# Kernel tuning notes

Measured on AMD Instinct MI355X. Metric: run time of the kernel, lower is better.

## Reference

```python
import jax, jax.numpy as jnp
import numpy as np

B = 8192      # batch
F = 20        # sparse features
V = 1000      # vocab per sparse feature
E = 32        # embedding dim
ND = 10       # dense features
IN0 = (F + ND) * E  # 960 total embed dim
T = 2         # tasks
K = 4         # task experts per task
S = 4         # shared experts
D = 512       # expert dim
H = 256       # tower hidden
TEMP = 2.0    # gate temperature
EPS = 1e-5    # batchnorm eps


def setup_inputs() -> dict:
    key = jax.random.key(0)
    ks = iter(jax.random.split(key, 64))
    n = lambda shape, s=0.02: jax.random.normal(next(ks), shape, dtype=jnp.float32) * s
    inp = {
        'sparse_features': jax.random.randint(next(ks), (B, F), 0, V, dtype=jnp.int32),
        'dense_features': jax.random.normal(next(ks), (B, ND), dtype=jnp.float32),
        'emb_tables': n((F, V, E), 0.05),
        'dense_W': n((ND, ND * E)),
        'dense_b': jnp.zeros((ND * E,), jnp.float32),
    }
    for i, ind in enumerate([IN0, D, D]):
        inp[f'l{i}_Wt'] = n((T, K, ind, D))
        inp[f'l{i}_bt'] = jnp.zeros((T, K, D), jnp.float32)
        inp[f'l{i}_Ws'] = n((S, ind, D))
        inp[f'l{i}_bs'] = jnp.zeros((S, D), jnp.float32)
        inp[f'l{i}_Wg'] = n((T, ind, K + S))
        inp[f'l{i}_bg'] = jnp.zeros((T, K + S), jnp.float32)
    inp['tw1'] = n((T, D, H)); inp['tb1'] = jnp.zeros((T, H), jnp.float32)
    inp['bn_g'] = jnp.ones((T, H), jnp.float32); inp['bn_b'] = jnp.zeros((T, H), jnp.float32)
    inp['bn_m'] = jnp.zeros((T, H), jnp.float32); inp['bn_v'] = jnp.ones((T, H), jnp.float32)
    inp['tw2'] = n((T, H, H // 2)); inp['tb2'] = jnp.zeros((T, H // 2), jnp.float32)
    inp['tw3'] = n((T, H // 2)); inp['tb3'] = jnp.zeros((T,), jnp.float32)
    return inp


def _ple_layer(x, Wt, bt, Ws, bs, Wg, bg):
    # x: [B, in]; Wt: [T,K,in,D]; Ws: [S,in,D]; Wg: [T,in,K+S]
    shared = jax.nn.relu(jnp.einsum('bi,sio->bso', x, Ws) + bs)        # [B,S,D]
    task = jax.nn.relu(jnp.einsum('bi,tkio->btko', x, Wt) + bt)        # [B,T,K,D]
    Bn = x.shape[0]
    stack = jnp.concatenate(
        [task, jnp.broadcast_to(shared[:, None], (Bn, T) + shared.shape[1:])], axis=2)  # [B,T,K+S,D]
    gw = jax.nn.softmax((jnp.einsum('bi,tie->bte', x, Wg) + bg) / TEMP, axis=-1)        # [B,T,K+S]
    return jnp.einsum('bte,bted->btd', gw, stack)                      # [B,T,D]


def reference(sparse_features, dense_features, emb_tables, dense_W, dense_b,
              l0_Wt, l0_bt, l0_Ws, l0_bs, l0_Wg, l0_bg,
              l1_Wt, l1_bt, l1_Ws, l1_bs, l1_Wg, l1_bg,
              l2_Wt, l2_bt, l2_Ws, l2_bs, l2_Wg, l2_bg,
              tw1, tb1, bn_g, bn_b, bn_m, bn_v, tw2, tb2, tw3, tb3):
    # embedding: per-feature table lookup then concat with projected dense
    sp = emb_tables[jnp.arange(F)[None, :], sparse_features]           # [B,F,E]
    embed = jnp.concatenate(
        [sp.reshape(sp.shape[0], F * E), dense_features @ dense_W + dense_b], axis=1)  # [B,IN0]

    x = embed
    tout = None
    for (Wt, bt, Ws, bs, Wg, bg) in [
        (l0_Wt, l0_bt, l0_Ws, l0_bs, l0_Wg, l0_bg),
        (l1_Wt, l1_bt, l1_Ws, l1_bs, l1_Wg, l1_bg),
        (l2_Wt, l2_bt, l2_Ws, l2_bs, l2_Wg, l2_bg),
    ]:
        tout = _ple_layer(x, Wt, bt, Ws, bs, Wg, bg)   # [B,T,D]
        x = tout.mean(axis=1)                           # next layer input

    # task towers (eval mode: BN uses running stats, dropout off)
    h = jnp.einsum('btd,tdh->bth', tout, tw1) + tb1
    h = (h - bn_m) / jnp.sqrt(bn_v + EPS) * bn_g + bn_b
    h = jax.nn.relu(h)
    h = jax.nn.relu(jnp.einsum('bth,thg->btg', h, tw2) + tb2)
    logits = jnp.einsum('btg,tg->bt', h, tw3) + tb3     # [B,T]

    ctr = jax.nn.sigmoid(logits[:, 0])
    cvr_raw = jax.nn.sigmoid(logits[:, 1])
    ctcvr = ctr * cvr_raw
    # use_esmm=True -> cvr_pred == ctcvr
    return jnp.stack([ctr, ctcvr, ctcvr])               # [3,B]: ctr, cvr, ctcvr
```

## Files before the change

kernel.cpp:

```cpp
#include <hip/hip_runtime.h>
#include <math.h>

#define Bn 8192
#define INP0 960
#define Dn 512
#define Hn 256
#define TEMP_INV 0.5f

typedef __attribute__((ext_vector_type(8))) short short8;
typedef __attribute__((ext_vector_type(8))) unsigned short ushort8;
typedef __attribute__((ext_vector_type(4))) float f32x4;

__device__ __forceinline__ int swz(int x) { return x ^ ((x >> 3) & 0x70); }
__device__ __forceinline__ int swz8(int x) { return x ^ (((x >> 7) & 3) << 3); }

__device__ __forceinline__ unsigned short f2bf(float f) {
  unsigned u = __builtin_bit_cast(unsigned, f);
  u += 0x7FFF + ((u >> 16) & 1);
  return (unsigned short)(u >> 16);
}
__device__ __forceinline__ float bf2f(unsigned short s) {
  unsigned u = ((unsigned)s) << 16;
  return __builtin_bit_cast(float, u);
}
__device__ __forceinline__ int pk4fp8(float a, float b, float c, float d) {
  int r = __builtin_amdgcn_cvt_pk_fp8_f32(a, b, 0, 0);
  r = __builtin_amdgcn_cvt_pk_fp8_f32(c, d, r, 1);
  return r;
}
__device__ __forceinline__ void gload16(const void* g, void* l) {
  __builtin_amdgcn_global_load_lds(
      (const __attribute__((address_space(1))) unsigned int*)g,
      (__attribute__((address_space(3))) unsigned int*)l, 16, 0, 0);
}

template <int IN>
__global__ __launch_bounds__(256) void conv_w(const float* __restrict__ Wt,
                                              const float* __restrict__ Ws,
                                              unsigned char* __restrict__ Wbt) {
  __shared__ float T[64][33];
  const int NK = IN / 32;
  int kk = blockIdx.x, dblk = blockIdx.y, e = blockIdx.z;
  int t = threadIdx.x;
  const float* base = (e < 8) ? (Wt + (size_t)e * IN * Dn) : (Ws + (size_t)(e - 8) * IN * Dn);
  int k = t >> 3, dq = t & 7;
  const float* gp = base + (size_t)(kk * 32 + k) * Dn + dblk * 64 + dq * 8;
  float4 v0 = *(const float4*)gp, v1 = *(const float4*)(gp + 4);
  T[dq * 8 + 0][k] = v0.x; T[dq * 8 + 1][k] = v0.y; T[dq * 8 + 2][k] = v0.z; T[dq * 8 + 3][k] = v0.w;
  T[dq * 8 + 4][k] = v1.x; T[dq * 8 + 5][k] = v1.y; T[dq * 8 + 6][k] = v1.z; T[dq * 8 + 7][k] = v1.w;
  __syncthreads();
  int L = t * 8;
  int nat = swz8(L);
  int c = nat >> 5, k0 = nat & 31;
  int2 o;
  o.x = pk4fp8(T[c][k0 + 0] * 16.f, T[c][k0 + 1] * 16.f, T[c][k0 + 2] * 16.f, T[c][k0 + 3] * 16.f);
  o.y = pk4fp8(T[c][k0 + 4] * 16.f, T[c][k0 + 5] * 16.f, T[c][k0 + 6] * 16.f, T[c][k0 + 7] * 16.f);
  *(int2*)(Wbt + (((size_t)(dblk * NK + kk) * 12 + e) << 11) + L) = o;
}

template <int K, int H>
__global__ __launch_bounds__(256) void conv_tw(const float* __restrict__ W,
                                               unsigned short* __restrict__ out) {
  __shared__ float T[64][33];
  int kk = blockIdx.x, hb = blockIdx.y, t = blockIdx.z;
  int tid = threadIdx.x;
  const float* base = W + (size_t)t * K * H;
  int k = tid >> 3, dq = tid & 7;
  const float* gp = base + (size_t)(kk * 32 + k) * H + hb * 64 + dq * 8;
  float4 v0 = *(const float4*)gp, v1 = *(const float4*)(gp + 4);
  T[dq * 8 + 0][k] = v0.x; T[dq * 8 + 1][k] = v0.y; T[dq * 8 + 2][k] = v0.z; T[dq * 8 + 3][k] = v0.w;
  T[dq * 8 + 4][k] = v1.x; T[dq * 8 + 5][k] = v1.y; T[dq * 8 + 6][k] = v1.z; T[dq * 8 + 7][k] = v1.w;
  __syncthreads();
  int L = tid * 16;
  int nat = swz(L);
  int c = nat >> 6, k0 = (nat & 63) >> 1;
  ushort8 o;
#pragma unroll
  for (int u = 0; u < 8; ++u) o[u] = f2bf(T[c][k0 + u]);
  const int NHB = H / 64;
  *(ushort8*)(out + (((size_t)(kk * NHB + hb) * 2 + t) << 11) + (L >> 1)) = o;
}

__global__ __launch_bounds__(256) void embed_kernel(
    const int* __restrict__ sparse, const float* __restrict__ dense,
    const float* __restrict__ emb, const float* __restrict__ dW,
    const float* __restrict__ db,
    unsigned short* __restrict__ xn, unsigned char* __restrict__ xt) {
  int b = blockIdx.x, t = threadIdx.x;
  __shared__ float dfs[10];
  if (t < 10) dfs[t] = dense[b * 10 + t];
  __syncthreads();
  if (t >= 240) return;
  int c = t * 4;
  float v[4];
  if (c < 640) {
    int f = c >> 5, e0 = c & 31;
    int idx = sparse[b * 20 + f];
    const float* ep = emb + ((size_t)f * 1000 + idx) * 32 + e0;
    float4 q = *(const float4*)ep;
    v[0] = q.x; v[1] = q.y; v[2] = q.z; v[3] = q.w;
  } else {
    int j = c - 640;
#pragma unroll
    for (int u = 0; u < 4; ++u) {
      float a = db[j + u];
#pragma unroll
      for (int d = 0; d < 10; ++d) a += dfs[d] * dW[d * 320 + j + u];
      v[u] = a;
    }
  }
  ushort4 pk;
  pk.x = f2bf(v[0]); pk.y = f2bf(v[1]); pk.z = f2bf(v[2]); pk.w = f2bf(v[3]);
  *(ushort4*)(xn + (size_t)b * 960 + c) = pk;
  int kk = c >> 5, bblk = b >> 6;
  int nat = ((b & 63) << 5) + (c & 31);
  int p8 = pk4fp8(v[0] * 16.f, v[1] * 16.f, v[2] * 16.f, v[3] * 16.f);
  *(int*)(xt + (((size_t)kk * 128 + bblk) << 11) + swz8(nat)) = p8;
}

template <int IN>
__global__ __launch_bounds__(256) void gate_kernel(
    const unsigned short* __restrict__ x, const float* __restrict__ Wg,
    const float* __restrict__ bg, float* __restrict__ gates) {
  int tid = threadIdx.x;
  int wv = tid >> 6, lane = tid & 63;
  int b = blockIdx.x * 4 + wv;
  int e = lane & 15, t = e >> 3, eg = e & 7;
  int slice = lane >> 4;
  const unsigned short* xr = x + (size_t)b * IN;
  const float* wr = Wg + (size_t)t * IN * 8 + eg;
  float p = 0.f;
  for (int i = slice * (IN / 4); i < (slice + 1) * (IN / 4); i += 4) {
    ushort4 xv = *(const ushort4*)(xr + i);
    p += bf2f(xv.x) * wr[(size_t)(i + 0) * 8];
    p += bf2f(xv.y) * wr[(size_t)(i + 1) * 8];
    p += bf2f(xv.z) * wr[(size_t)(i + 2) * 8];
    p += bf2f(xv.w) * wr[(size_t)(i + 3) * 8];
  }
  p += __shfl_xor(p, 32);
  p += __shfl_xor(p, 16);
  float z = (p + bg[t * 8 + eg]) * TEMP_INV;
  float m = z;
  m = fmaxf(m, __shfl_xor(m, 1)); m = fmaxf(m, __shfl_xor(m, 2)); m = fmaxf(m, __shfl_xor(m, 4));
  float ex = expf(z - m);
  float s = ex;
  s += __shfl_xor(s, 1); s += __shfl_xor(s, 2); s += __shfl_xor(s, 4);
  if (lane < 16) gates[(size_t)b * 16 + lane] = ex / s;
}

#define GSH 0
#define OUTS 4096
#define SB 22528
#define STG 26624

template <int IN, int MODE>
__global__ __launch_bounds__(768, 3) void ple_mfma(
    const unsigned char* __restrict__ xt, const float* __restrict__ gates,
    const unsigned char* __restrict__ Wbt,
    const float* __restrict__ btb, const float* __restrict__ bsh,
    unsigned short* __restrict__ outn, unsigned char* __restrict__ outt8,
    unsigned short* __restrict__ outtb) {
  __shared__ __align__(16) char smem[102400];
  const int NKv = IN / 32;
  int tid = threadIdx.x;
  int wv = tid >> 6, lane = tid & 63;
  int r = lane & 15, g = lane >> 4;
  int s = blockIdx.x;
  int dblk = s & 7, bblk = s >> 3;
  int b0 = bblk * 64, d0 = dblk * 64;

  if (tid < 256)
    *(float4*)(smem + GSH + tid * 16) = *(const float4*)(gates + (size_t)b0 * 16 + tid * 4);

  f32x4 acc[4][4];
#pragma unroll
  for (int i = 0; i < 4; ++i)
#pragma unroll
    for (int j = 0; j < 4; ++j) acc[i][j] = f32x4{0.f, 0.f, 0.f, 0.f};

  const unsigned char* xchunk = xt + ((size_t)bblk << 11);
  const unsigned char* wchunk = Wbt + ((size_t)(dblk * NKv) * 12 << 11);

  auto stage = [&](int t, char* lb) {
    const unsigned char* ws = wchunk + (size_t)t * 24576;
    gload16(ws + tid * 16, lb + tid * 16);
    gload16(ws + tid * 16 + 12288, lb + tid * 16 + 12288);
    if (tid < 128)
      gload16(xchunk + (size_t)t * (128 * 2048) + tid * 16, lb + 24576 + tid * 16);
  };

  stage(0, smem + SB);
  stage(1, smem + SB + STG);

  for (int kk = 0; kk < NKv; ++kk) {
    if (kk == NKv - 1) {
      asm volatile("s_waitcnt vmcnt(0)" ::: "memory");
    } else if (tid < 128) {
      asm volatile("s_waitcnt vmcnt(3)" ::: "memory");
    } else {
      asm volatile("s_waitcnt vmcnt(2)" ::: "memory");
    }
    __builtin_amdgcn_s_barrier();
    {
      const char* lb = smem + SB + (kk % 3) * STG;
      const char* xb = lb + 24576;
      const char* wb = lb + (wv << 11);
      long A[4], B[4];
#pragma unroll
      for (int rt = 0; rt < 4; ++rt)
        A[rt] = *(const long*)(xb + swz8(((rt * 16 + r) << 5) + (g << 3)));
#pragma unroll
      for (int ct = 0; ct < 4; ++ct)
        B[ct] = *(const long*)(wb + swz8(((ct * 16 + r) << 5) + (g << 3)));
#pragma unroll
      for (int rt = 0; rt < 4; ++rt)
#pragma unroll
        for (int ct = 0; ct < 4; ++ct)
          acc[rt][ct] = __builtin_amdgcn_mfma_f32_16x16x32_fp8_fp8(A[rt], B[ct], acc[rt][ct], 0, 0, 0);
    }
    if (kk + 2 < NKv) stage(kk + 2, smem + SB + ((kk + 2) % 3) * STG);
  }
  __syncthreads();

  {
    const float* bp = (wv < 8) ? (btb + wv * Dn) : (bsh + (wv - 8) * Dn);
    float bias[4];
#pragma unroll
    for (int ct = 0; ct < 4; ++ct) bias[ct] = bp[d0 + ct * 16 + r];
    char* ex = smem + SB + (wv << 12);
#pragma unroll
    for (int rt = 0; rt < 4; ++rt)
#pragma unroll
      for (int ct = 0; ct < 4; ++ct) {
        float v0 = fmaxf(acc[rt][ct][0] * 0.00390625f + bias[ct], 0.f) * 16.f;
        float v1 = fmaxf(acc[rt][ct][1] * 0.00390625f + bias[ct], 0.f) * 16.f;
        float v2 = fmaxf(acc[rt][ct][2] * 0.00390625f + bias[ct], 0.f) * 16.f;
        float v3 = fmaxf(acc[rt][ct][3] * 0.00390625f + bias[ct], 0.f) * 16.f;
        int col = ct * 16 + r;
        int off = (col << 6) + rt * 16 + g * 4;
        off ^= (col & 7) << 3;
        *(int*)(ex + off) = pk4fp8(v0, v1, v2, v3);
      }
  }
  __syncthreads();

  if (tid < 512) {
    int col = tid & 63, q = tid >> 6;
    int exoff = ((col << 6) + (q << 3)) ^ ((col & 7) << 3);
    long v[12];
#pragma unroll
    for (int e = 0; e < 12; ++e)
      v[e] = *(const long*)(smem + SB + (e << 12) + exoff);
    unsigned short* os0 = (unsigned short*)(smem + OUTS);
    unsigned short* os1 = os0 + 64 * 72;
#pragma unroll
    for (int half = 0; half < 2; ++half) {
#pragma unroll
      for (int jj = 0; jj < 4; ++jj) {
        int row = (q << 3) + half * 4 + jj;
        const float* gp = (const float*)(smem + GSH + (row << 6));
        float4 ga = ((const float4*)gp)[0];
        float4 gb = ((const float4*)gp)[1];
        float4 gc = ((const float4*)gp)[2];
        float4 gd = ((const float4*)gp)[3];
        float f[12];
#pragma unroll
        for (int e = 0; e < 12; ++e) {
          unsigned w32 = (unsigned)(v[e] >> (half * 32));
          f[e] = __builtin_amdgcn_cvt_f32_fp8((int)(w32 >> (jj * 8)), 0);
        }
        float s0 = ga.x * f[0] + ga.y * f[1] + ga.z * f[2] + ga.w * f[3] +
                   gb.x * f[8] + gb.y * f[9] + gb.z * f[10] + gb.w * f[11];
        float s1 = gc.x * f[4] + gc.y * f[5] + gc.z * f[6] + gc.w * f[7] +
                   gd.x * f[8] + gd.y * f[9] + gd.z * f[10] + gd.w * f[11];
        os0[row * 72 + col] = f2bf(s0 * 0.0625f);
        os1[row * 72 + col] = f2bf(s1 * 0.0625f);
      }
    }
  }
  __syncthreads();

  if (tid < 512) {
    int row = tid >> 3, cq = tid & 7;
    const unsigned short* os0 = (const unsigned short*)(smem + OUTS) + row * 72 + cq * 8;
    const unsigned short* os1 = os0 + 64 * 72;
    ushort8 p0 = *(const ushort8*)os0, p1 = *(const ushort8*)os1;
    int b = b0 + row, d = d0 + cq * 8;
    int kk2 = d >> 5;
    if (MODE == 0) {
      float m[8];
      ushort8 pk;
#pragma unroll
      for (int u = 0; u < 8; ++u) {
        m[u] = 0.5f * (bf2f((unsigned short)p0[u]) + bf2f((unsigned short)p1[u]));
        pk[u] = f2bf(m[u]);
      }
      *(ushort8*)(outn + (size_t)b * Dn + d) = pk;
      int nat = (row << 5) + (d & 31);
      int2 o8;
      o8.x = pk4fp8(m[0] * 16.f, m[1] * 16.f, m[2] * 16.f, m[3] * 16.f);
      o8.y = pk4fp8(m[4] * 16.f, m[5] * 16.f, m[6] * 16.f, m[7] * 16.f);
      *(int2*)(outt8 + (((size_t)kk2 * 128 + bblk) << 11) + swz8(nat)) = o8;
    } else {
      int nat = (row << 6) + ((d & 31) << 1);
      *(ushort8*)(outtb + (((size_t)(0 * 16 + kk2) * 128 + bblk) << 11) + (swz(nat) >> 1)) = p0;
      *(ushort8*)(outtb + (((size_t)(1 * 16 + kk2) * 128 + bblk) << 11) + (swz(nat) >> 1)) = p1;
    }
  }
}

#define TWBUF 36864
#define H1OFF 73728

__global__ __launch_bounds__(512) void tower_mfma(
    const unsigned short* __restrict__ toutT,
    const unsigned short* __restrict__ twbt1, const unsigned short* __restrict__ twbt2,
    const float* __restrict__ tb1,
    const float* __restrict__ bng, const float* __restrict__ bnb,
    const float* __restrict__ bnm, const float* __restrict__ bnv,
    const float* __restrict__ tb2, const float* __restrict__ tw3,
    const float* __restrict__ tb3, float* __restrict__ out) {
  __shared__ __align__(16) char smem[106496];
  int tid = threadIdx.x;
  int wv = tid >> 6, lane = tid & 63, r = lane & 15, g = lane >> 4;
  int blk = blockIdx.x;
  int bblk = blk >> 1, sub = blk & 1;
  int b0 = blk * 32;
  char* h1t = smem + H1OFF;

  int t1 = wv >> 2, hb = wv & 3;
  f32x4 acc[2][4];
#pragma unroll
  for (int i = 0; i < 2; ++i)
#pragma unroll
    for (int j = 0; j < 4; ++j) acc[i][j] = f32x4{0.f, 0.f, 0.f, 0.f};

  auto stage1 = [&](int t, char* lb) {
#pragma unroll
    for (int i = 0; i < 4; ++i)
      gload16((const char*)twbt1 + (size_t)t * 32768 + tid * 16 + i * 8192,
              lb + tid * 16 + i * 8192);
    if (tid < 256) {
      int tt = tid >> 7, off = (tid & 127) * 16;
      gload16((const char*)toutT + (((size_t)(tt * 16 + t) * 128 + bblk) << 12) + sub * 2048 + off,
              lb + 32768 + tt * 2048 + off);
    }
  };

  stage1(0, smem);
  __syncthreads();
  int cur = 0;
  for (int kk = 0; kk < 16; ++kk) {
    if (kk + 1 < 16) stage1(kk + 1, smem + (cur ^ 1) * TWBUF);
    {
      const char* lb = smem + cur * TWBUF;
      const char* wb = lb + (hb * 2 + t1) * 4096;
      const char* xb = lb + 32768 + t1 * 2048;
      short8 a[2], bfr[4];
#pragma unroll
      for (int rt = 0; rt < 2; ++rt)
        a[rt] = *(const short8*)(xb + swz(((rt * 16 + r) << 6) + (g << 4)));
#pragma unroll
      for (int ct = 0; ct < 4; ++ct)
        bfr[ct] = *(const short8*)(wb + swz(((ct * 16 + r) << 6) + (g << 4)));
#pragma unroll
      for (int rt = 0; rt < 2; ++rt)
#pragma unroll
        for (int ct = 0; ct < 4; ++ct)
          acc[rt][ct] = __builtin_amdgcn_mfma_f32_16x16x32_bf16(a[rt], bfr[ct], acc[rt][ct], 0, 0, 0);
    }
    __syncthreads();
    cur ^= 1;
  }

  {
#pragma unroll
    for (int ct = 0; ct < 4; ++ct) {
      int h = hb * 64 + ct * 16 + r;
      int idx = t1 * 256 + h;
      float inv = rsqrtf(bnv[idx] + 1e-5f) * bng[idx];
      float mu = bnm[idx], be = bnb[idx], bias = tb1[idx];
      int kk2 = h >> 5, kloc = h & 31;
      char* tile = h1t + (t1 * 8 + kk2) * 2048;
#pragma unroll
      for (int rt = 0; rt < 2; ++rt)
#pragma unroll
        for (int j = 0; j < 4; ++j) {
          int lr = rt * 16 + g * 4 + j;
          float v = acc[rt][ct][j] + bias;
          v = (v - mu) * inv + be;
          v = fmaxf(v, 0.f);
          *(unsigned short*)(tile + swz((lr << 6) + (kloc << 1))) = f2bf(v);
        }
    }
  }
  __syncthreads();

  float* h2x = (float*)smem;
  if (wv < 4) {
    int t2 = wv >> 1, hb2 = wv & 1;
    f32x4 acc2[2][4];
#pragma unroll
    for (int i = 0; i < 2; ++i)
#pragma unroll
      for (int j = 0; j < 4; ++j) acc2[i][j] = f32x4{0.f, 0.f, 0.f, 0.f};
    for (int kk = 0; kk < 8; ++kk) {
      const char* xb = h1t + (t2 * 8 + kk) * 2048;
      const char* wb = (const char*)twbt2 + ((kk * 2 + hb2) * 2 + t2) * 4096;
      short8 a[2], bfr[4];
#pragma unroll
      for (int rt = 0; rt < 2; ++rt)
        a[rt] = *(const short8*)(xb + swz(((rt * 16 + r) << 6) + (g << 4)));
#pragma unroll
      for (int ct = 0; ct < 4; ++ct)
        bfr[ct] = *(const short8*)(wb + swz(((ct * 16 + r) << 6) + (g << 4)));
#pragma unroll
      for (int rt = 0; rt < 2; ++rt)
#pragma unroll
        for (int ct = 0; ct < 4; ++ct)
          acc2[rt][ct] = __builtin_amdgcn_mfma_f32_16x16x32_bf16(a[rt], bfr[ct], acc2[rt][ct], 0, 0, 0);
    }
#pragma unroll
    for (int ct = 0; ct < 4; ++ct) {
      int col = hb2 * 64 + ct * 16 + r;
      float bias = tb2[t2 * 128 + col];
#pragma unroll
      for (int rt = 0; rt < 2; ++rt)
#pragma unroll
        for (int j = 0; j < 4; ++j) {
          int lr = rt * 16 + g * 4 + j;
          h2x[(t2 * 32 + lr) * 129 + col] = fmaxf(acc2[rt][ct][j] + bias, 0.f);
        }
    }
  }
  __syncthreads();

  float* lgs = (float*)(smem + 40960);
  if (tid < 64) {
    int t3 = tid >> 5, lr = tid & 31;
    const float* hr = h2x + (t3 * 32 + lr) * 129;
    const float* w3 = tw3 + t3 * 128;
    float s = 0.f;
#pragma unroll 8
    for (int i = 0; i < 128; ++i) s += hr[i] * w3[i];
    lgs[t3 * 32 + lr] = s + tb3[t3];
  }
  __syncthreads();
  if (tid < 32) {
    int b = b0 + tid;
    float ctr = 1.f / (1.f + expf(-lgs[tid]));
    float cvr = 1.f / (1.f + expf(-lgs[32 + tid]));
    float cc = ctr * cvr;
    out[b] = ctr;
    out[Bn + b] = cc;
    out[2 * Bn + b] = cc;
  }
}

extern "C" void kernel_launch(void* const* d_in, const int* in_sizes, int n_in,
                              void* d_out, int out_size, void* d_ws, size_t ws_size,
                              hipStream_t stream) {
  const int* sparse   = (const int*)d_in[0];
  const float* dense  = (const float*)d_in[1];
  const float* emb    = (const float*)d_in[2];
  const float* dW     = (const float*)d_in[3];
  const float* db     = (const float*)d_in[4];
  const float* Wt[3]  = {(const float*)d_in[5],  (const float*)d_in[11], (const float*)d_in[17]};
  const float* btb[3] = {(const float*)d_in[6],  (const float*)d_in[12], (const float*)d_in[18]};
  const float* Wsh[3] = {(const float*)d_in[7],  (const float*)d_in[13], (const float*)d_in[19]};
  const float* bsh[3] = {(const float*)d_in[8],  (const float*)d_in[14], (const float*)d_in[20]};
  const float* Wg[3]  = {(const float*)d_in[9],  (const float*)d_in[15], (const float*)d_in[21]};
  const float* bg[3]  = {(const float*)d_in[10], (const float*)d_in[16], (const float*)d_in[22]};
  const float* tw1 = (const float*)d_in[23];
  const float* tb1 = (const float*)d_in[24];
  const float* bng = (const float*)d_in[25];
  const float* bnb = (const float*)d_in[26];
  const float* bnm = (const float*)d_in[27];
  const float* bnv = (const float*)d_in[28];
  const float* tw2 = (const float*)d_in[29];
  const float* tb2 = (const float*)d_in[30];
  const float* tw3 = (const float*)d_in[31];
  const float* tb3 = (const float*)d_in[32];

  unsigned short* x0n = (unsigned short*)d_ws;
  unsigned short* x1n = x0n + (size_t)Bn * 960;
  unsigned short* toutT = x1n + (size_t)Bn * 512;
  float* gatesB = (float*)(toutT + (size_t)Bn * 1024);
  unsigned short* twbt1 = (unsigned short*)(gatesB + (size_t)Bn * 16);
  unsigned short* twbt2 = twbt1 + (size_t)2 * 512 * 256;
  unsigned char* x0t = (unsigned char*)(twbt2 + (size_t)2 * 256 * 128);
  unsigned char* x1t = x0t + (size_t)Bn * 960;
  unsigned char* Wbt = x1t + (size_t)Bn * 512;
  unsigned short* x2n = x0n;
  unsigned char* x2t = x0t;

  conv_tw<512, 256><<<dim3(16, 4, 2), 256, 0, stream>>>(tw1, twbt1);
  conv_tw<256, 128><<<dim3(8, 2, 2), 256, 0, stream>>>(tw2, twbt2);

  conv_w<960><<<dim3(30, 8, 12), 256, 0, stream>>>(Wt[0], Wsh[0], Wbt);
  embed_kernel<<<Bn, 256, 0, stream>>>(sparse, dense, emb, dW, db, x0n, x0t);
  gate_kernel<960><<<Bn / 4, 256, 0, stream>>>(x0n, Wg[0], bg[0], gatesB);
  ple_mfma<960, 0><<<1024, 768, 0, stream>>>(x0t, gatesB, Wbt, btb[0], bsh[0], x1n, x1t, nullptr);

  conv_w<512><<<dim3(16, 8, 12), 256, 0, stream>>>(Wt[1], Wsh[1], Wbt);
  gate_kernel<512><<<Bn / 4, 256, 0, stream>>>(x1n, Wg[1], bg[1], gatesB);
  ple_mfma<512, 0><<<1024, 768, 0, stream>>>(x1t, gatesB, Wbt, btb[1], bsh[1], x2n, x2t, nullptr);

  conv_w<512><<<dim3(16, 8, 12), 256, 0, stream>>>(Wt[2], Wsh[2], Wbt);
  gate_kernel<512><<<Bn / 4, 256, 0, stream>>>(x2n, Wg[2], bg[2], gatesB);
  ple_mfma<512, 1><<<1024, 768, 0, stream>>>(x2t, gatesB, Wbt, btb[2], bsh[2], nullptr, nullptr, toutT);

  tower_mfma<<<256, 512, 0, stream>>>(toutT, twbt1, twbt2, tb1, bng, bnb, bnm, bnv,
                                      tb2, tw3, tb3, (float*)d_out);
}
```

Before: 315.8 us.

## Double K-tile to 64 with new FP8 swizzled layout and double buffering

Changes the FP8 packed layout of activations and weights to 64-wide K chunks with a new XOR swizzle, so each MFMA lane loads 16 bytes at once. The PLE GEMM then handles two 16x16x32 MFMA steps per barrier. The three-stage prefetch pipeline becomes a two-stage one that issues the next stage after the barrier. This halves the number of loop iterations and barriers, at the cost of more LDS per block and a full vmcnt(0) wait on every iteration.

```diff
diff --git a/kernel.cpp b/kernel.cpp
--- a/kernel.cpp
+++ b/kernel.cpp
@@ -10,9 +10,9 @@
 typedef __attribute__((ext_vector_type(8))) short short8;
 typedef __attribute__((ext_vector_type(8))) unsigned short ushort8;
 typedef __attribute__((ext_vector_type(4))) float f32x4;
+typedef __attribute__((ext_vector_type(2))) long lx2;
 
 __device__ __forceinline__ int swz(int x) { return x ^ ((x >> 3) & 0x70); }
-__device__ __forceinline__ int swz8(int x) { return x ^ (((x >> 7) & 3) << 3); }
 
 __device__ __forceinline__ unsigned short f2bf(float f) {
   unsigned u = __builtin_bit_cast(unsigned, f);
@@ -38,24 +38,31 @@
 __global__ __launch_bounds__(256) void conv_w(const float* __restrict__ Wt,
                                               const float* __restrict__ Ws,
                                               unsigned char* __restrict__ Wbt) {
-  __shared__ float T[64][33];
-  const int NK = IN / 32;
+  __shared__ float T[64][65];
+  const int NK = IN / 64;
   int kk = blockIdx.x, dblk = blockIdx.y, e = blockIdx.z;
   int t = threadIdx.x;
   const float* base = (e < 8) ? (Wt + (size_t)e * IN * Dn) : (Ws + (size_t)(e - 8) * IN * Dn);
-  int k = t >> 3, dq = t & 7;
-  const float* gp = base + (size_t)(kk * 32 + k) * Dn + dblk * 64 + dq * 8;
-  float4 v0 = *(const float4*)gp, v1 = *(const float4*)(gp + 4);
-  T[dq * 8 + 0][k] = v0.x; T[dq * 8 + 1][k] = v0.y; T[dq * 8 + 2][k] = v0.z; T[dq * 8 + 3][k] = v0.w;
-  T[dq * 8 + 4][k] = v1.x; T[dq * 8 + 5][k] = v1.y; T[dq * 8 + 6][k] = v1.z; T[dq * 8 + 7][k] = v1.w;
-  __syncthreads();
-  int L = t * 8;
-  int nat = swz8(L);
-  int c = nat >> 5, k0 = nat & 31;
-  int2 o;
-  o.x = pk4fp8(T[c][k0 + 0] * 16.f, T[c][k0 + 1] * 16.f, T[c][k0 + 2] * 16.f, T[c][k0 + 3] * 16.f);
-  o.y = pk4fp8(T[c][k0 + 4] * 16.f, T[c][k0 + 5] * 16.f, T[c][k0 + 6] * 16.f, T[c][k0 + 7] * 16.f);
-  *(int2*)(Wbt + (((size_t)(dblk * NK + kk) * 12 + e) << 11) + L) = o;
+  int k = t >> 2, dg = t & 3;
+  const float* gp = base + (size_t)(kk * 64 + k) * Dn + dblk * 64 + dg * 16;
+#pragma unroll
+  for (int i = 0; i < 4; ++i) {
+    float4 v = *(const float4*)(gp + i * 4);
+    T[dg * 16 + i * 4 + 0][k] = v.x;
+    T[dg * 16 + i * 4 + 1][k] = v.y;
+    T[dg * 16 + i * 4 + 2][k] = v.z;
+    T[dg * 16 + i * 4 + 3][k] = v.w;
+  }
+  __syncthreads();
+  int col = t >> 2, gq = t & 3;
+  int g = gq ^ ((col >> 1) & 3);
+  const float* Tc = T[col];
+  int4 o;
+  o.x = pk4fp8(Tc[g * 8 + 0] * 16.f, Tc[g * 8 + 1] * 16.f, Tc[g * 8 + 2] * 16.f, Tc[g * 8 + 3] * 16.f);
+  o.y = pk4fp8(Tc[g * 8 + 4] * 16.f, Tc[g * 8 + 5] * 16.f, Tc[g * 8 + 6] * 16.f, Tc[g * 8 + 7] * 16.f);
+  o.z = pk4fp8(Tc[32 + g * 8 + 0] * 16.f, Tc[32 + g * 8 + 1] * 16.f, Tc[32 + g * 8 + 2] * 16.f, Tc[32 + g * 8 + 3] * 16.f);
+  o.w = pk4fp8(Tc[32 + g * 8 + 4] * 16.f, Tc[32 + g * 8 + 5] * 16.f, Tc[32 + g * 8 + 6] * 16.f, Tc[32 + g * 8 + 7] * 16.f);
+  *(int4*)(Wbt + (((size_t)(dblk * NK + kk) * 12 + e) << 12) + t * 16) = o;
 }
 
 template <int K, int H>
@@ -112,10 +119,13 @@
   ushort4 pk;
   pk.x = f2bf(v[0]); pk.y = f2bf(v[1]); pk.z = f2bf(v[2]); pk.w = f2bf(v[3]);
   *(ushort4*)(xn + (size_t)b * 960 + c) = pk;
-  int kk = c >> 5, bblk = b >> 6;
-  int nat = ((b & 63) << 5) + (c & 31);
+  int col = b & 63;
+  int lc = c & 63;
+  int ks = lc >> 5, g = (lc & 31) >> 3, j0 = lc & 7;
+  int gq = g ^ ((col >> 1) & 3);
+  int pos = (col << 6) + (gq << 4) + (ks << 3) + j0;
   int p8 = pk4fp8(v[0] * 16.f, v[1] * 16.f, v[2] * 16.f, v[3] * 16.f);
-  *(int*)(xt + (((size_t)kk * 128 + bblk) << 11) + swz8(nat)) = p8;
+  *(int*)(xt + (((size_t)(c >> 6) * 128 + (b >> 6)) << 12) + pos) = p8;
 }
 
 template <int IN>
@@ -151,7 +161,7 @@
 #define GSH 0
 #define OUTS 4096
 #define SB 22528
-#define STG 26624
+#define STG 53248
 
 template <int IN, int MODE>
 __global__ __launch_bounds__(768, 3) void ple_mfma(
@@ -160,8 +170,8 @@
     const float* __restrict__ btb, const float* __restrict__ bsh,
     unsigned short* __restrict__ outn, unsigned char* __restrict__ outt8,
     unsigned short* __restrict__ outtb) {
-  __shared__ __align__(16) char smem[102400];
-  const int NKv = IN / 32;
+  __shared__ __align__(16) char smem[129024];
+  const int NK = IN / 64;
   int tid = threadIdx.x;
   int wv = tid >> 6, lane = tid & 63;
   int r = lane & 15, g = lane >> 4;
@@ -178,47 +188,45 @@
 #pragma unroll
     for (int j = 0; j < 4; ++j) acc[i][j] = f32x4{0.f, 0.f, 0.f, 0.f};
 
-  const unsigned char* xchunk = xt + ((size_t)bblk << 11);
-  const unsigned char* wchunk = Wbt + ((size_t)(dblk * NKv) * 12 << 11);
+  const unsigned char* xchunk = xt + ((size_t)bblk << 12);
+  const unsigned char* wchunk = Wbt + (size_t)(dblk * NK) * 49152;
 
   auto stage = [&](int t, char* lb) {
-    const unsigned char* ws = wchunk + (size_t)t * 24576;
-    gload16(ws + tid * 16, lb + tid * 16);
-    gload16(ws + tid * 16 + 12288, lb + tid * 16 + 12288);
-    if (tid < 128)
-      gload16(xchunk + (size_t)t * (128 * 2048) + tid * 16, lb + 24576 + tid * 16);
+    const unsigned char* ws = wchunk + (size_t)t * 49152;
+#pragma unroll
+    for (int i = 0; i < 4; ++i)
+      gload16(ws + tid * 16 + i * 12288, lb + tid * 16 + i * 12288);
+    if (tid < 256)
+      gload16(xchunk + (size_t)t * (128 * 4096) + tid * 16, lb + 49152 + tid * 16);
   };
 
   stage(0, smem + SB);
-  stage(1, smem + SB + STG);
-
-  for (int kk = 0; kk < NKv; ++kk) {
-    if (kk == NKv - 1) {
-      asm volatile("s_waitcnt vmcnt(0)" ::: "memory");
-    } else if (tid < 128) {
-      asm volatile("s_waitcnt vmcnt(3)" ::: "memory");
-    } else {
-      asm volatile("s_waitcnt vmcnt(2)" ::: "memory");
-    }
+
+  for (int kk = 0; kk < NK; ++kk) {
+    asm volatile("s_waitcnt vmcnt(0)" ::: "memory");
     __builtin_amdgcn_s_barrier();
+    if (kk + 1 < NK) stage(kk + 1, smem + SB + ((kk + 1) & 1) * STG);
     {
-      const char* lb = smem + SB + (kk % 3) * STG;
-      const char* xb = lb + 24576;
-      const char* wb = lb + (wv << 11);
-      long A[4], B[4];
+      const char* lb = smem + SB + (kk & 1) * STG;
+      const char* xb = lb + 49152;
+      const char* wb = lb + (wv << 12);
+      int base = (r << 6) + ((g ^ ((r >> 1) & 3)) << 4);
+      lx2 A[4], B[4];
+#pragma unroll
+      for (int rt = 0; rt < 4; ++rt) A[rt] = *(const lx2*)(xb + rt * 1024 + base);
+#pragma unroll
+      for (int ct = 0; ct < 4; ++ct) B[ct] = *(const lx2*)(wb + ct * 1024 + base);
 #pragma unroll
       for (int rt = 0; rt < 4; ++rt)
-        A[rt] = *(const long*)(xb + swz8(((rt * 16 + r) << 5) + (g << 3)));
-#pragma unroll
-      for (int ct = 0; ct < 4; ++ct)
-        B[ct] = *(const long*)(wb + swz8(((ct * 16 + r) << 5) + (g << 3)));
+#pragma unroll
+        for (int ct = 0; ct < 4; ++ct)
+          acc[rt][ct] = __builtin_amdgcn_mfma_f32_16x16x32_fp8_fp8(A[rt][0], B[ct][0], acc[rt][ct], 0, 0, 0);
 #pragma unroll
       for (int rt = 0; rt < 4; ++rt)
 #pragma unroll
         for (int ct = 0; ct < 4; ++ct)
-          acc[rt][ct] = __builtin_amdgcn_mfma_f32_16x16x32_fp8_fp8(A[rt], B[ct], acc[rt][ct], 0, 0, 0);
-    }
-    if (kk + 2 < NKv) stage(kk + 2, smem + SB + ((kk + 2) % 3) * STG);
+          acc[rt][ct] = __builtin_amdgcn_mfma_f32_16x16x32_fp8_fp8(A[rt][1], B[ct][1], acc[rt][ct], 0, 0, 0);
+    }
   }
   __syncthreads();
 
@@ -286,7 +294,6 @@
     const unsigned short* os1 = os0 + 64 * 72;
     ushort8 p0 = *(const ushort8*)os0, p1 = *(const ushort8*)os1;
     int b = b0 + row, d = d0 + cq * 8;
-    int kk2 = d >> 5;
     if (MODE == 0) {
       float m[8];
       ushort8 pk;
@@ -296,12 +303,16 @@
         pk[u] = f2bf(m[u]);
       }
       *(ushort8*)(outn + (size_t)b * Dn + d) = pk;
-      int nat = (row << 5) + (d & 31);
+      int lk = d & 63;
+      int ks = lk >> 5, g2 = (lk & 31) >> 3;
+      int gq = g2 ^ ((row >> 1) & 3);
+      int pos = (row << 6) + (gq << 4) + (ks << 3);
       int2 o8;
       o8.x = pk4fp8(m[0] * 16.f, m[1] * 16.f, m[2] * 16.f, m[3] * 16.f);
       o8.y = pk4fp8(m[4] * 16.f, m[5] * 16.f, m[6] * 16.f, m[7] * 16.f);
-      *(int2*)(outt8 + (((size_t)kk2 * 128 + bblk) << 11) + swz8(nat)) = o8;
+      *(int2*)(outt8 + (((size_t)dblk * 128 + bblk) << 12) + pos) = o8;
     } else {
+      int kk2 = d >> 5;
       int nat = (row << 6) + ((d & 31) << 1);
       *(ushort8*)(outtb + (((size_t)(0 * 16 + kk2) * 128 + bblk) << 11) + (swz(nat) >> 1)) = p0;
       *(ushort8*)(outtb + (((size_t)(1 * 16 + kk2) * 128 + bblk) << 11) + (swz(nat) >> 1)) = p1;
@@ -497,16 +508,16 @@
   conv_tw<512, 256><<<dim3(16, 4, 2), 256, 0, stream>>>(tw1, twbt1);
   conv_tw<256, 128><<<dim3(8, 2, 2), 256, 0, stream>>>(tw2, twbt2);
 
-  conv_w<960><<<dim3(30, 8, 12), 256, 0, stream>>>(Wt[0], Wsh[0], Wbt);
+  conv_w<960><<<dim3(15, 8, 12), 256, 0, stream>>>(Wt[0], Wsh[0], Wbt);
   embed_kernel<<<Bn, 256, 0, stream>>>(sparse, dense, emb, dW, db, x0n, x0t);
   gate_kernel<960><<<Bn / 4, 256, 0, stream>>>(x0n, Wg[0], bg[0], gatesB);
   ple_mfma<960, 0><<<1024, 768, 0, stream>>>(x0t, gatesB, Wbt, btb[0], bsh[0], x1n, x1t, nullptr);
 
-  conv_w<512><<<dim3(16, 8, 12), 256, 0, stream>>>(Wt[1], Wsh[1], Wbt);
+  conv_w<512><<<dim3(8, 8, 12), 256, 0, stream>>>(Wt[1], Wsh[1], Wbt);
   gate_kernel<512><<<Bn / 4, 256, 0, stream>>>(x1n, Wg[1], bg[1], gatesB);
   ple_mfma<512, 0><<<1024, 768, 0, stream>>>(x1t, gatesB, Wbt, btb[1], bsh[1], x2n, x2t, nullptr);
 
-  conv_w<512><<<dim3(16, 8, 12), 256, 0, stream>>>(Wt[2], Wsh[2], Wbt);
+  conv_w<512><<<dim3(8, 8, 12), 256, 0, stream>>>(Wt[2], Wsh[2], Wbt);
   gate_kernel<512><<<Bn / 4, 256, 0, stream>>>(x2n, Wg[2], bg[2], gatesB);
   ple_mfma<512, 1><<<1024, 768, 0, stream>>>(x2t, gatesB, Wbt, btb[2], bsh[2], nullptr, nullptr, toutT);
 
```

Result: faster. 296.7 us (-6.1%).
